# Kernel optimization log

Hardware: AMD Instinct MI355X
Metric: run time of the kernel (lower is better)

## Reference

```python
import jax, jax.numpy as jnp
import numpy as np

B, CIN, COUT, H, W = 8, 256, 256, 64, 64


def setup_inputs() -> dict:
    key = jax.random.key(0)
    k1, k2, k3 = jax.random.split(key, 3)
    x = jax.random.normal(k1, (B, CIN, H, W), dtype=jnp.float32)
    style = jax.random.normal(k2, (B, CIN), dtype=jnp.float32)
    # kaiming_normal_ (fan_in = CIN*3*3, gain = sqrt(2))
    fan_in = CIN * 9
    weight = jax.random.normal(k3, (COUT, CIN, 3, 3), dtype=jnp.float32) * np.sqrt(2.0 / fan_in)
    return {"x": x, "style": style, "weight": weight}


def reference(x, style, weight):
    b, cin, h, w = x.shape
    cout = weight.shape[0]
    # modulate: [B, Cout, Cin, 3, 3]
    mw = style[:, None, :, None, None] * weight[None]
    # demodulate
    sigma = jnp.sqrt(jnp.sum(mw * mw, axis=(2, 3, 4), keepdims=True) + 1e-8)
    dw = mw / sigma
    # per-sample conv via grouped convolution (groups = B)
    x_g = x.reshape(1, b * cin, h, w)
    w_g = dw.reshape(b * cout, cin, 3, 3)
    out = jax.lax.conv_general_dilated(
        x_g, w_g,
        window_strides=(1, 1),
        padding=((1, 1), (1, 1)),
        feature_group_count=b,
        dimension_numbers=("NCHW", "OIHW", "NCHW"),
    )
    return out.reshape(b, cout, h, w)
```

## Files before the change

kernel.cpp:

```cpp
#include <hip/hip_runtime.h>

#define B_ 8
#define CIN_ 256
#define COUT_ 256

typedef short short8_t __attribute__((ext_vector_type(8)));
typedef float float4_t __attribute__((ext_vector_type(4)));

#define DWA_SHORTS   (B_ * 9 * 32 * COUT_ * 8)
#define XPRE_SHORTS  (B_ * 8 * 66 * 66 * 32)

__device__ __forceinline__ unsigned short f2bf(float f) {
    union { float f; unsigned u; } v; v.f = f;
    unsigned u = v.u;
    unsigned r = (u + 0x7fffu + ((u >> 16) & 1u)) >> 16;
    return (unsigned short)r;
}

__global__ __launch_bounds__(256) void k_xpre(const float* __restrict__ x,
                                              unsigned short* __restrict__ xpre) {
    const int h_out = blockIdx.x;
    const int cb = blockIdx.y, b = blockIdx.z;
    const int t = threadIdx.x;
    const int h_in = h_out - 1;
    unsigned short* dst_row = xpre + (((size_t)(b * 8 + cb) * 66 + h_out)) * 66 * 32;
#pragma unroll
    for (int pass = 0; pass < 2; ++pass) {
        int p = t + pass * 256;
        if (p >= 264) break;
        int w_out = p >> 2, g = p & 3;
        int w_in = w_out - 1;
        short8_t v = (short8_t){0, 0, 0, 0, 0, 0, 0, 0};
        if ((unsigned)h_in < 64u && (unsigned)w_in < 64u) {
            const float* xp = x + (((size_t)(b * CIN_ + cb * 32 + g * 8)) * 64 + h_in) * 64 + w_in;
#pragma unroll
            for (int j = 0; j < 8; ++j) v[j] = (short)f2bf(xp[(size_t)j * 4096]);
        }
        *(short8_t*)(dst_row + (size_t)w_out * 32 + g * 8) = v;
    }
}

__global__ __launch_bounds__(256) void k_modulate(const float* __restrict__ weight,
                                                  const float* __restrict__ style,
                                                  unsigned short* __restrict__ dwA) {
    __shared__ float wlds[4 * 2304];
    const int t = threadIdx.x;
    const int co0 = blockIdx.x * 4;
    const int co_l = t >> 6;
    const int lane = t & 63;
    const int co = co0 + co_l;

    const float* wp = weight + (size_t)co0 * 2304;
#pragma unroll
    for (int k = 0; k < 36; ++k) wlds[t + 256 * k] = wp[t + 256 * k];
    __syncthreads();

    float wv[4][9];
    float ss[4];
#pragma unroll
    for (int k = 0; k < 4; ++k) {
        float a = 0.f;
#pragma unroll
        for (int tap = 0; tap < 9; ++tap) {
            float w = wlds[co_l * 2304 + (lane + 64 * k) * 9 + tap];
            wv[k][tap] = w;
            a += w * w;
        }
        ss[k] = a;
    }
    float sv[8][4];
#pragma unroll
    for (int b = 0; b < 8; ++b)
#pragma unroll
        for (int k = 0; k < 4; ++k) sv[b][k] = style[b * CIN_ + lane + 64 * k];

    float inv[8];
#pragma unroll
    for (int b = 0; b < 8; ++b) {
        float part = 0.f;
#pragma unroll
        for (int k = 0; k < 4; ++k) part += sv[b][k] * sv[b][k] * ss[k];
#pragma unroll
        for (int off = 32; off > 0; off >>= 1) part += __shfl_xor(part, off, 64);
        inv[b] = 1.0f / sqrtf(part + 1e-8f);
    }

    const size_t base = (size_t)co * 8 + (lane & 7) + (size_t)(lane >> 3) * 2048;
#pragma unroll
    for (int b = 0; b < 8; ++b)
#pragma unroll
        for (int tap = 0; tap < 9; ++tap)
#pragma unroll
            for (int k = 0; k < 4; ++k) {
                size_t addr = ((size_t)(b * 9 + tap) * 32 + k * 8) * 2048 + base;
                dwA[addr] = f2bf(wv[k][tap] * sv[b][k] * inv[b]);
            }
}

__global__ __launch_bounds__(256) void k_conv(const unsigned short* __restrict__ xpre,
                                              const unsigned short* __restrict__ dwA,
                                              float* __restrict__ out) {
    __shared__ __align__(16) unsigned short xs[2][4 * 66 * 40];

    const int rowgrp = blockIdx.x;
    const int co_tile = blockIdx.y;
    const int b = blockIdx.z;
    const int tid = threadIdx.x;
    const int lane = tid & 63, wid = tid >> 6;
    const int wave_m = wid >> 1, wave_n = wid & 1;
    const int quad = lane >> 4, l16 = lane & 15;
    const int r0 = rowgrp * 2;
    const int co_base = co_tile * 128 + wave_m * 64;

    float4_t acc[4][4];
#pragma unroll
    for (int mi = 0; mi < 4; ++mi)
#pragma unroll
        for (int ni = 0; ni < 4; ++ni) acc[mi][ni] = (float4_t){0.f, 0.f, 0.f, 0.f};

    short8_t st[5];
    auto load_regs = [&](int cb) {
        const unsigned short* s = xpre + ((size_t)((b * 8 + cb) * 66 + r0)) * 2112;
#pragma unroll
        for (int it = 0; it < 4; ++it)
            st[it] = *(const short8_t*)(s + (size_t)(tid + it * 256) * 8);
        if (tid < 32) st[4] = *(const short8_t*)(s + (size_t)(tid + 1024) * 8);
    };
    auto store_lds = [&](int buf) {
        unsigned short* d = xs[buf];
#pragma unroll
        for (int it = 0; it < 4; ++it) {
            int c = tid + it * 256;
            *(short8_t*)(d + (c >> 2) * 40 + (c & 3) * 8) = st[it];
        }
        if (tid < 32) {
            int c = tid + 1024;
            *(short8_t*)(d + (c >> 2) * 40 + (c & 3) * 8) = st[4];
        }
    };

    short8_t abuf[3][4];
    auto loadA = [&](short8_t* dst, int acb, int atap) {
        const unsigned short* Ab = dwA + ((size_t)(b * 9 + atap) * 32 + acb * 4 + quad) * 2048;
#pragma unroll
        for (int mi = 0; mi < 4; ++mi)
            dst[mi] = *(const short8_t*)(Ab + (co_base + mi * 16 + l16) * 8);
    };

    load_regs(0);
    loadA(abuf[0], 0, 0);
    loadA(abuf[1], 0, 1);

    for (int cb = 0; cb < 8; ++cb) {
        store_lds(cb & 1);
        __syncthreads();
        if (cb < 7) load_regs(cb + 1);

        const unsigned short* xb = xs[cb & 1];
#pragma unroll
        for (int tap = 0; tap < 9; ++tap) {
            const int nl = tap + 2;
            const int acb = cb + nl / 9, atap = nl % 9;
            if (acb < 8) loadA(abuf[nl % 3], acb, atap);

            const int dh = tap / 3, dwc = tap % 3;
            const unsigned short* brow = xb + (wave_n + dh) * 66 * 40;
            short8_t bf[4];
#pragma unroll
            for (int ni = 0; ni < 4; ++ni)
                bf[ni] = *(const short8_t*)(brow + (ni * 16 + l16 + dwc) * 40 + quad * 8);

            const short8_t* ac = abuf[tap % 3];
#pragma unroll
            for (int mi = 0; mi < 4; ++mi)
#pragma unroll
                for (int ni = 0; ni < 4; ++ni)
                    acc[mi][ni] = __builtin_amdgcn_mfma_f32_16x16x32_bf16(
                        ac[mi], bf[ni], acc[mi][ni], 0, 0, 0);
        }
    }

    const int orow = r0 + wave_n;
#pragma unroll
    for (int mi = 0; mi < 4; ++mi)
#pragma unroll
        for (int ni = 0; ni < 4; ++ni)
#pragma unroll
            for (int r = 0; r < 4; ++r) {
                int co = co_base + mi * 16 + quad * 4 + r;
                int c = ni * 16 + l16;
                out[(((size_t)b * COUT_ + co) * 64 + orow) * 64 + c] = acc[mi][ni][r];
            }
}

extern "C" void kernel_launch(void* const* d_in, const int* in_sizes, int n_in,
                              void* d_out, int out_size, void* d_ws, size_t ws_size,
                              hipStream_t stream) {
    const float* x = (const float*)d_in[0];
    const float* style = (const float*)d_in[1];
    const float* weight = (const float*)d_in[2];
    float* out = (float*)d_out;

    unsigned short* dwA = (unsigned short*)d_ws;
    unsigned short* xpre = dwA + DWA_SHORTS;

    k_xpre<<<dim3(66, 8, B_), 256, 0, stream>>>(x, xpre);
    k_modulate<<<dim3(64), 256, 0, stream>>>(weight, style, dwA);
    k_conv<<<dim3(32, 2, B_), 256, 0, stream>>>(xpre, dwA, out);
}
```

Before: 141.1 us.

## Merge prep kernels, stage input via direct global-to-LDS loads with swizzle, enlarge conv tile

```diff
diff --git a/kernel.cpp b/kernel.cpp
--- a/kernel.cpp
+++ b/kernel.cpp
@@ -17,52 +17,58 @@
     return (unsigned short)r;
 }
 
-__global__ __launch_bounds__(256) void k_xpre(const float* __restrict__ x,
-                                              unsigned short* __restrict__ xpre) {
-    const int h_out = blockIdx.x;
-    const int cb = blockIdx.y, b = blockIdx.z;
+__device__ __forceinline__ void gload_lds16(const unsigned short* g, unsigned short* l) {
+    __builtin_amdgcn_global_load_lds(
+        (__attribute__((address_space(1))) void*)(g),
+        (__attribute__((address_space(3))) void*)(l), 16, 0, 0);
+}
+
+__global__ __launch_bounds__(256) void k_prep(const float* __restrict__ x,
+                                              const float* __restrict__ style,
+                                              const float* __restrict__ weight,
+                                              unsigned short* __restrict__ xpre,
+                                              unsigned short* __restrict__ dwA) {
+    const int blk = blockIdx.x;
     const int t = threadIdx.x;
-    const int h_in = h_out - 1;
-    unsigned short* dst_row = xpre + (((size_t)(b * 8 + cb) * 66 + h_out)) * 66 * 32;
-#pragma unroll
-    for (int pass = 0; pass < 2; ++pass) {
-        int p = t + pass * 256;
-        if (p >= 264) break;
-        int w_out = p >> 2, g = p & 3;
-        int w_in = w_out - 1;
-        short8_t v = (short8_t){0, 0, 0, 0, 0, 0, 0, 0};
-        if ((unsigned)h_in < 64u && (unsigned)w_in < 64u) {
-            const float* xp = x + (((size_t)(b * CIN_ + cb * 32 + g * 8)) * 64 + h_in) * 64 + w_in;
-#pragma unroll
-            for (int j = 0; j < 8; ++j) v[j] = (short)f2bf(xp[(size_t)j * 4096]);
+
+    if (blk >= 64) {
+        const int e = blk - 64;
+        const int h_out = e % 66;
+        const int q2 = e / 66;
+        const int cb = q2 & 7, b = q2 >> 3;
+        const int h_in = h_out - 1;
+        unsigned short* dst_row = xpre + ((size_t)(b * 8 + cb) * 66 + h_out) * 66 * 32;
+#pragma unroll
+        for (int pass = 0; pass < 2; ++pass) {
+            int p = t + pass * 256;
+            if (p >= 264) break;
+            int w_out = p >> 2, g = p & 3;
+            int w_in = w_out - 1;
+            short8_t v = (short8_t){0, 0, 0, 0, 0, 0, 0, 0};
+            if ((unsigned)h_in < 64u && (unsigned)w_in < 64u) {
+                const float* xp = x + (((size_t)(b * CIN_ + cb * 32 + g * 8)) * 64 + h_in) * 64 + w_in;
+#pragma unroll
+                for (int j = 0; j < 8; ++j) v[j] = (short)f2bf(xp[(size_t)j * 4096]);
+            }
+            const int chunk = g ^ ((w_out >> 1) & 3);
+            *(short8_t*)(dst_row + (size_t)w_out * 32 + chunk * 8) = v;
         }
-        *(short8_t*)(dst_row + (size_t)w_out * 32 + g * 8) = v;
-    }
-}
-
-__global__ __launch_bounds__(256) void k_modulate(const float* __restrict__ weight,
-                                                  const float* __restrict__ style,
-                                                  unsigned short* __restrict__ dwA) {
-    __shared__ float wlds[4 * 2304];
-    const int t = threadIdx.x;
-    const int co0 = blockIdx.x * 4;
+        return;
+    }
+
     const int co_l = t >> 6;
     const int lane = t & 63;
-    const int co = co0 + co_l;
-
-    const float* wp = weight + (size_t)co0 * 2304;
-#pragma unroll
-    for (int k = 0; k < 36; ++k) wlds[t + 256 * k] = wp[t + 256 * k];
-    __syncthreads();
+    const int co = blk * 4 + co_l;
 
     float wv[4][9];
     float ss[4];
+    const float* wp = weight + (size_t)co * 2304;
 #pragma unroll
     for (int k = 0; k < 4; ++k) {
         float a = 0.f;
 #pragma unroll
         for (int tap = 0; tap < 9; ++tap) {
-            float w = wlds[co_l * 2304 + (lane + 64 * k) * 9 + tap];
+            float w = wp[(lane + 64 * k) * 9 + tap];
             wv[k][tap] = w;
             a += w * w;
         }
@@ -97,100 +103,104 @@
             }
 }
 
-__global__ __launch_bounds__(256) void k_conv(const unsigned short* __restrict__ xpre,
-                                              const unsigned short* __restrict__ dwA,
-                                              float* __restrict__ out) {
-    __shared__ __align__(16) unsigned short xs[2][4 * 66 * 40];
-
-    const int rowgrp = blockIdx.x;
-    const int co_tile = blockIdx.y;
-    const int b = blockIdx.z;
+__global__ __launch_bounds__(256, 1) void k_conv(const unsigned short* __restrict__ xpre,
+                                                 const unsigned short* __restrict__ dwA,
+                                                 float* __restrict__ out) {
+    __shared__ __align__(16) unsigned short xs[2][4 * 66 * 32];
+
+    const int b = blockIdx.x;
+    const int rowgrp = blockIdx.y;
     const int tid = threadIdx.x;
     const int lane = tid & 63, wid = tid >> 6;
     const int wave_m = wid >> 1, wave_n = wid & 1;
     const int quad = lane >> 4, l16 = lane & 15;
     const int r0 = rowgrp * 2;
-    const int co_base = co_tile * 128 + wave_m * 64;
-
-    float4_t acc[4][4];
-#pragma unroll
-    for (int mi = 0; mi < 4; ++mi)
+    const int co_base = wave_m * 128;
+
+    float4_t acc[8][4];
+#pragma unroll
+    for (int mi = 0; mi < 8; ++mi)
 #pragma unroll
         for (int ni = 0; ni < 4; ++ni) acc[mi][ni] = (float4_t){0.f, 0.f, 0.f, 0.f};
 
-    short8_t st[5];
-    auto load_regs = [&](int cb) {
-        const unsigned short* s = xpre + ((size_t)((b * 8 + cb) * 66 + r0)) * 2112;
-#pragma unroll
-        for (int it = 0; it < 4; ++it)
-            st[it] = *(const short8_t*)(s + (size_t)(tid + it * 256) * 8);
-        if (tid < 32) st[4] = *(const short8_t*)(s + (size_t)(tid + 1024) * 8);
+    const unsigned short* src_base = xpre + (size_t)b * 8 * 66 * 66 * 32;
+
+    auto stage = [&](int cb, int buf) {
+        const unsigned short* s = src_base + ((size_t)cb * 66 + r0) * 2112;
+        unsigned short* d = xs[buf];
+#pragma unroll
+        for (int k = 0; k < 4; ++k)
+            gload_lds16(s + (size_t)(tid + k * 256) * 8, d + (size_t)(tid + k * 256) * 8);
+        if (tid < 32)
+            gload_lds16(s + (size_t)(tid + 1024) * 8, d + (size_t)(tid + 1024) * 8);
     };
-    auto store_lds = [&](int buf) {
-        unsigned short* d = xs[buf];
-#pragma unroll
-        for (int it = 0; it < 4; ++it) {
-            int c = tid + it * 256;
-            *(short8_t*)(d + (c >> 2) * 40 + (c & 3) * 8) = st[it];
-        }
-        if (tid < 32) {
-            int c = tid + 1024;
-            *(short8_t*)(d + (c >> 2) * 40 + (c & 3) * 8) = st[4];
+
+    short8_t abuf[2][8];
+    auto loadA = [&](short8_t* dst, int acb, int atap) {
+        const unsigned short* Ab = dwA + ((size_t)(b * 9 + atap) * 32 + acb * 4 + quad) * 2048
+                                       + (size_t)(co_base + l16) * 8;
+#pragma unroll
+        for (int mi = 0; mi < 8; ++mi)
+            dst[mi] = *(const short8_t*)(Ab + mi * 128);
+    };
+
+    short8_t bf[2][4];
+    auto readB = [&](short8_t* dst, const unsigned short* xb, int tap) {
+        const int dh = tap / 3, dwc = tap % 3;
+        const unsigned short* brow = xb + (wave_n + dh) * (66 * 32);
+#pragma unroll
+        for (int ni = 0; ni < 4; ++ni) {
+            const int col = ni * 16 + l16 + dwc;
+            dst[ni] = *(const short8_t*)(brow + col * 32 + (quad ^ ((col >> 1) & 3)) * 8);
         }
     };
 
-    short8_t abuf[3][4];
-    auto loadA = [&](short8_t* dst, int acb, int atap) {
-        const unsigned short* Ab = dwA + ((size_t)(b * 9 + atap) * 32 + acb * 4 + quad) * 2048;
-#pragma unroll
-        for (int mi = 0; mi < 4; ++mi)
-            dst[mi] = *(const short8_t*)(Ab + (co_base + mi * 16 + l16) * 8);
-    };
-
-    load_regs(0);
+#define TAP_BLOCK(CBV, PAR)                                                   \
+    do {                                                                      \
+        const unsigned short* xb_ = xs[(PAR)];                                \
+        readB(bf[0], xb_, 0);                                                 \
+        _Pragma("unroll")                                                     \
+        for (int tap = 0; tap < 9; ++tap) {                                   \
+            if (tap < 8) {                                                    \
+                loadA(abuf[((PAR) + tap + 1) & 1], (CBV), tap + 1);           \
+                readB(bf[(tap + 1) & 1], xb_, tap + 1);                       \
+            } else if ((CBV) < 7) {                                           \
+                loadA(abuf[((PAR) + 1) & 1], (CBV) + 1, 0);                   \
+            }                                                                 \
+            const short8_t* ac = abuf[((PAR) + tap) & 1];                     \
+            const short8_t* bc = bf[tap & 1];                                 \
+            _Pragma("unroll")                                                 \
+            for (int mi = 0; mi < 8; ++mi)                                    \
+                _Pragma("unroll")                                             \
+                for (int ni = 0; ni < 4; ++ni)                                \
+                    acc[mi][ni] = __builtin_amdgcn_mfma_f32_16x16x32_bf16(    \
+                        ac[mi], bc[ni], acc[mi][ni], 0, 0, 0);                \
+        }                                                                     \
+    } while (0)
+
+    stage(0, 0);
     loadA(abuf[0], 0, 0);
-    loadA(abuf[1], 0, 1);
-
-    for (int cb = 0; cb < 8; ++cb) {
-        store_lds(cb & 1);
+
+    for (int cb2 = 0; cb2 < 4; ++cb2) {
+        const int cbA = cb2 * 2, cbB = cbA + 1;
         __syncthreads();
-        if (cb < 7) load_regs(cb + 1);
-
-        const unsigned short* xb = xs[cb & 1];
-#pragma unroll
-        for (int tap = 0; tap < 9; ++tap) {
-            const int nl = tap + 2;
-            const int acb = cb + nl / 9, atap = nl % 9;
-            if (acb < 8) loadA(abuf[nl % 3], acb, atap);
-
-            const int dh = tap / 3, dwc = tap % 3;
-            const unsigned short* brow = xb + (wave_n + dh) * 66 * 40;
-            short8_t bf[4];
-#pragma unroll
-            for (int ni = 0; ni < 4; ++ni)
-                bf[ni] = *(const short8_t*)(brow + (ni * 16 + l16 + dwc) * 40 + quad * 8);
-
-            const short8_t* ac = abuf[tap % 3];
-#pragma unroll
-            for (int mi = 0; mi < 4; ++mi)
-#pragma unroll
-                for (int ni = 0; ni < 4; ++ni)
-                    acc[mi][ni] = __builtin_amdgcn_mfma_f32_16x16x32_bf16(
-                        ac[mi], bf[ni], acc[mi][ni], 0, 0, 0);
-        }
-    }
+        stage(cbB, 1);
+        TAP_BLOCK(cbA, 0);
+        __syncthreads();
+        if (cbB < 7) stage(cbB + 1, 0);
+        TAP_BLOCK(cbB, 1);
+    }
+#undef TAP_BLOCK
 
     const int orow = r0 + wave_n;
-#pragma unroll
-    for (int mi = 0; mi < 4; ++mi)
+    float* outp = out + ((size_t)b * COUT_ + co_base) * 4096 + (size_t)orow * 64;
+#pragma unroll
+    for (int mi = 0; mi < 8; ++mi)
 #pragma unroll
         for (int ni = 0; ni < 4; ++ni)
 #pragma unroll
-            for (int r = 0; r < 4; ++r) {
-                int co = co_base + mi * 16 + quad * 4 + r;
-                int c = ni * 16 + l16;
-                out[(((size_t)b * COUT_ + co) * 64 + orow) * 64 + c] = acc[mi][ni][r];
-            }
+            for (int r = 0; r < 4; ++r)
+                outp[(size_t)(mi * 16 + quad * 4 + r) * 4096 + ni * 16 + l16] = acc[mi][ni][r];
 }
 
 extern "C" void kernel_launch(void* const* d_in, const int* in_sizes, int n_in,
@@ -204,7 +214,6 @@
     unsigned short* dwA = (unsigned short*)d_ws;
     unsigned short* xpre = dwA + DWA_SHORTS;
 
-    k_xpre<<<dim3(66, 8, B_), 256, 0, stream>>>(x, xpre);
-    k_modulate<<<dim3(64), 256, 0, stream>>>(weight, style, dwA);
-    k_conv<<<dim3(32, 2, B_), 256, 0, stream>>>(xpre, dwA, out);
-}
+    k_prep<<<dim3(64 + B_ * 8 * 66), 256, 0, stream>>>(x, style, weight, xpre, dwA);
+    k_conv<<<dim3(8, 32), 256, 0, stream>>>(xpre, dwA, out);
+}
```

New measurement: 213.6 us. +51.3%, slower.
